# Optimization experiments

Hardware: AMD Instinct MI355X
Metric: run time of the kernel (lower is better)

## Reference

```python
import jax, jax.numpy as jnp
import numpy as np
from jax import lax

# pywt Wavelet('db3') analysis filters (dec_lo, dec_hi)
DEC_LO = jnp.array([0.035226291882100656, -0.08544127388224149, -0.13501102001039084,
                    0.4598775021193313, 0.8068915093133388, 0.3326705529509569], dtype=jnp.float32)
DEC_HI = jnp.array([-0.3326705529509569, 0.8068915093133388, -0.4598775021193313,
                    -0.13501102001039084, 0.08544127388224149, 0.035226291882100656], dtype=jnp.float32)


def _dwt_level(x):
    # One analysis level of pytorch_wavelets DWT1D with mode='zero'.
    # x: [B, N] -> (lo, hi) each [B, (N+L-1)//2]
    N = x.shape[-1]
    L = DEC_LO.shape[0]
    outsize = (N + L - 1) // 2  # pywt.dwt_coeff_len, zero mode
    p = 2 * (outsize - 1) - N + L
    # conv_general_dilated does cross-correlation; reversed filter == true convolution
    w = jnp.stack([DEC_LO[::-1], DEC_HI[::-1]])[:, None, :]  # [2, 1, L]
    y = lax.conv_general_dilated(x[:, None, :], w, window_strides=(2,),
                                 padding=[(p // 2, p - p // 2)])  # [B, 2, outsize]
    return y[:, 0, :], y[:, 1, :]


def _wavelet_features(sig, level=3):
    # sig: [B, N]. Returns (mean of final low-pass, sum over levels of ||hf||_2) per row.
    lo = sig
    high = jnp.zeros(sig.shape[0], sig.dtype)
    for _ in range(level):
        lo, hi = _dwt_level(lo)
        high = high + jnp.sqrt(jnp.sum(hi * hi, axis=-1))
    return jnp.mean(lo, axis=-1), high


def _dirichlet_weight(low, high):
    # Deterministic surrogate: Dirichlet([a1*10, a2*10]) has mean a1/(a1+a2),
    # replacing scipy dirichlet.rvs sampling with its expectation.
    a1 = jnp.clip(low, 1e-6)
    a2 = jnp.clip(high, 1e-6)
    return a1 / (a1 + a2)


def _forward(user_idx, item_idx, values, num_users, num_items):
    # item popularity: scatter-add of values * log1p(interaction count), L2-normalized
    counts = jnp.zeros(num_items, jnp.float32).at[item_idx].add(1.0)
    log_counts = jnp.log1p(counts)
    pop = jnp.zeros(num_items, jnp.float32).at[item_idx].add(values * log_counts[item_idx])
    pop = pop / (jnp.linalg.norm(pop) + 1e-8)
    # user activity
    act = jnp.zeros(num_users, jnp.float32).at[user_idx].add(
        values / jnp.log1p(pop[item_idx] + 1e-8))
    act = act / (jnp.linalg.norm(act) + 1e-8)
    # dense per-entity interaction signals (batched scatter replaces per-entity masking loop)
    user_sig = jnp.zeros((num_users, num_items), jnp.float32).at[user_idx, item_idx].add(values)
    user_sig = user_sig * (1.0 + act)[:, None]
    item_sig = jnp.zeros((num_items, num_users), jnp.float32).at[item_idx, user_idx].add(values)
    item_sig = item_sig * (1.0 + pop)[:, None]
    u_low, u_high = _wavelet_features(user_sig)
    i_low, i_high = _wavelet_features(item_sig)
    u_pop = _dirichlet_weight(u_low, u_high)
    i_pop = _dirichlet_weight(i_low, i_high)
    u_ni, i_ni = 1.0 - u_pop, 1.0 - i_pop
    wu_p, wu_n = u_pop[user_idx], u_ni[user_idx]
    wi_p, wi_n = i_pop[item_idx], i_ni[item_idx]
    # nnz-valued sparse outputs: [UIPG(=pop/pop), UING(=niche/niche), pop/niche, niche/pop]
    return jnp.stack([values * wu_p * wi_p,
                      values * wu_n * wi_n,
                      values * wu_p * wi_n,
                      values * wu_n * wi_p])


def setup_inputs():
    key = jax.random.key(0)
    k1, k2, k3 = jax.random.split(key, 3)
    NNZ, U, I = 2_000_000, 8192, 8192
    return {
        "user_idx": jax.random.randint(k1, (NNZ,), 0, U, dtype=jnp.int32),
        "item_idx": jax.random.randint(k2, (NNZ,), 0, I, dtype=jnp.int32),
        "values": jax.random.uniform(k3, (NNZ,), dtype=jnp.float32),
        "num_users": U,
        "num_items": I,
    }


def reference(user_idx, item_idx, values, num_users, num_items):
    return _forward(user_idx, item_idx, values, num_users, num_items)
```

## Files before the change

kernel.cpp:

```cpp
#include <hip/hip_runtime.h>
#include <math.h>

#define NE 8192
#define HT 1024
#define NCH 8
#define RT 512
#define NROWS 16

__device__ __constant__ float LO_R[6] = {
    0.3326705529509569f, 0.8068915093133388f, 0.4598775021193313f,
    -0.13501102001039084f, -0.08544127388224149f, 0.035226291882100656f};
__device__ __constant__ float HI_RV[6] = {
    0.035226291882100656f, 0.08544127388224149f, -0.13501102001039084f,
    -0.4598775021193313f, 0.8068915093133388f, -0.3326705529509569f};

__device__ __forceinline__ float4 blockReduce4(float a, float b, float c, float d,
                                               float (*red)[4]) {
    #pragma unroll
    for (int off = 32; off > 0; off >>= 1) {
        a += __shfl_down(a, off); b += __shfl_down(b, off);
        c += __shfl_down(c, off); d += __shfl_down(d, off);
    }
    int lane = threadIdx.x & 63, wid = threadIdx.x >> 6;
    if (lane == 0) { red[wid][0] = a; red[wid][1] = b; red[wid][2] = c; red[wid][3] = d; }
    __syncthreads();
    float4 r = make_float4(0.f, 0.f, 0.f, 0.f);
    if (threadIdx.x == 0) {
        int nw = blockDim.x >> 6;
        for (int w = 0; w < nw; ++w) {
            r.x += red[w][0]; r.y += red[w][1]; r.z += red[w][2]; r.w += red[w][3];
        }
    }
    return r;
}

__device__ __forceinline__ float blockReduceSum(float v, float* red) {
    #pragma unroll
    for (int off = 32; off > 0; off >>= 1) v += __shfl_down(v, off);
    int lane = threadIdx.x & 63, wid = threadIdx.x >> 6;
    if (lane == 0) red[wid] = v;
    __syncthreads();
    float r = 0.f;
    if (threadIdx.x == 0) {
        int nw = blockDim.x >> 6;
        for (int i = 0; i < nw; ++i) r += red[i];
    }
    return r;
}

__global__ void k_tables(float* __restrict__ resp, float4* __restrict__ Tdiag) {
    int a = blockIdx.x * blockDim.x + threadIdx.x;
    if (a >= NE) return;
    float lo1r[8], hi1r[8];
    int k1a = max(0, (a >> 1) - 3);
    #pragma unroll
    for (int t = 0; t < 8; ++t) {
        int k = k1a + t;
        int j = a - 2 * k + 4;
        bool ok = (j >= 0 && j <= 5 && k <= 4097);
        lo1r[t] = ok ? LO_R[j] : 0.f;
        hi1r[t] = ok ? HI_RV[j] : 0.f;
    }
    float lo2r[8], hi2r[8];
    int k2a = max(0, (k1a >> 1) - 1);
    #pragma unroll
    for (int t = 0; t < 8; ++t) {
        int k = k2a + t;
        float aL = 0.f, aH = 0.f;
        if (k <= 2050) {
            #pragma unroll
            for (int j = 0; j < 6; ++j) {
                int idx = 2 * k - 4 + j - k1a;
                if (idx >= 0 && idx < 8) {
                    aL = fmaf(LO_R[j], lo1r[idx], aL);
                    aH = fmaf(HI_RV[j], lo1r[idx], aH);
                }
            }
        }
        lo2r[t] = aL; hi2r[t] = aH;
    }
    float lo3r[8], hi3r[8];
    int k3a = max(0, (k2a >> 1) - 1);
    #pragma unroll
    for (int t = 0; t < 8; ++t) {
        int k = k3a + t;
        float aL = 0.f, aH = 0.f;
        if (k <= 1027) {
            #pragma unroll
            for (int j = 0; j < 6; ++j) {
                int idx = 2 * k - 4 + j - k2a;
                if (idx >= 0 && idx < 8) {
                    aL = fmaf(LO_R[j], lo2r[idx], aL);
                    aH = fmaf(HI_RV[j], lo2r[idx], aH);
                }
            }
        }
        lo3r[t] = aL; hi3r[t] = aH;
    }
    float g1 = 0.f, g2 = 0.f, g3 = 0.f, w3 = 0.f;
    #pragma unroll
    for (int t = 0; t < 8; ++t) {
        g1 = fmaf(hi1r[t], hi1r[t], g1);
        g2 = fmaf(hi2r[t], hi2r[t], g2);
        g3 = fmaf(hi3r[t], hi3r[t], g3);
        w3 += lo3r[t];
    }
    Tdiag[a] = make_float4(w3, g1, g2, g3);
    float* rp = resp + (size_t)a * 32;
    #pragma unroll
    for (int t = 0; t < 8; ++t) { rp[t] = hi1r[t]; rp[8 + t] = hi2r[t]; rp[16 + t] = hi3r[t]; }
    rp[24] = __int_as_float(k1a);
    rp[25] = __int_as_float(k2a);
    rp[26] = __int_as_float(k3a);
}

__global__ void k_gram(const float* __restrict__ resp, float* __restrict__ Gt) {
    int idx = blockIdx.x * 256 + threadIdx.x;
    if (idx >= NE * 35) return;
    int a = idx / 35;
    int d = idx - a * 35 + 1;
    int b = a + d;
    float v1 = 0.f, v2 = 0.f, v3 = 0.f;
    const float* ra = resp + (size_t)a * 32;
    if (b < NE) {
        const float* rb = resp + (size_t)b * 32;
        {
            int s = __float_as_int(rb[26]) - __float_as_int(ra[26]);
            #pragma unroll
            for (int u = 0; u < 8; ++u) {
                int t = u + s;
                if (t >= 0 && t < 8) v3 = fmaf(rb[16 + u], ra[16 + t], v3);
            }
        }
        if (d <= 15) {
            int s = __float_as_int(rb[25]) - __float_as_int(ra[25]);
            #pragma unroll
            for (int u = 0; u < 8; ++u) {
                int t = u + s;
                if (t >= 0 && t < 8) v2 = fmaf(rb[8 + u], ra[8 + t], v2);
            }
        }
        if (d <= 5) {
            int s = __float_as_int(rb[24]) - __float_as_int(ra[24]);
            #pragma unroll
            for (int u = 0; u < 8; ++u) {
                int t = u + s;
                if (t >= 0 && t < 8) v1 = fmaf(rb[u], ra[t], v1);
            }
        }
    }
    float* g = Gt + (size_t)a * 56;
    if (d <= 5)  g[d - 1] = v1;
    if (d <= 15) g[5 + d - 1] = v2;
    g[20 + d - 1] = v3;
}

__global__ __launch_bounds__(HT) void k_hist3(const int* __restrict__ ui,
                                              const int* __restrict__ ii,
                                              const float* __restrict__ v, int nnz,
                                              int* __restrict__ sliceU,
                                              int* __restrict__ sliceI,
                                              float* __restrict__ sliceS) {
    __shared__ int hU[NE];
    __shared__ int hI[NE];
    __shared__ float hS[NE];
    int b = blockIdx.x, tid = threadIdx.x, hb = gridDim.x;
    int4* hU4 = (int4*)hU; int4* hI4 = (int4*)hI; int4* hS4 = (int4*)hS;
    int4 z4 = make_int4(0, 0, 0, 0);
    for (int j = tid; j < NE / 4; j += HT) { hU4[j] = z4; hI4[j] = z4; hS4[j] = z4; }
    __syncthreads();
    int C = (nnz + hb - 1) / hb;
    int beg = b * C, end = min(nnz, beg + C);
    for (int n = beg + tid; n < end; n += HT) {
        atomicAdd(&hU[ui[n]], 1);
        int it = ii[n];
        atomicAdd(&hI[it], 1);
        atomicAdd(&hS[it], v[n]);
    }
    __syncthreads();
    size_t base = (size_t)b * NE;
    int4* sU = (int4*)(sliceU + base); int4* sI = (int4*)(sliceI + base);
    int4* sS = (int4*)(sliceS + base);
    for (int j = tid; j < NE / 4; j += HT) { sU[j] = hU4[j]; sI[j] = hI4[j]; sS[j] = hS4[j]; }
}

__global__ void k_chunksum3(const int* __restrict__ sliceU, const int* __restrict__ sliceI,
                            const float* __restrict__ sliceS, int spc,
                            int* __restrict__ csU, int* __restrict__ csI,
                            float* __restrict__ csS) {
    int i = blockIdx.x * 256 + threadIdx.x;
    int c = blockIdx.y;
    int b0 = c * spc;
    int cu = 0, ci = 0; float sv = 0.f;
    for (int b = b0; b < b0 + spc; ++b) {
        size_t o = (size_t)b * NE + i;
        cu += sliceU[o]; ci += sliceI[o]; sv += sliceS[o];
    }
    size_t oc = (size_t)c * NE + i;
    csU[oc] = cu; csI[oc] = ci; csS[oc] = sv;
}

__global__ void k_final3(const int* __restrict__ csU, const int* __restrict__ csI,
                         const float* __restrict__ csS,
                         int* cntU, int* cntI, float* popraw, float* normAcc) {
    __shared__ float red[4];
    int i = blockIdx.x * 256 + threadIdx.x;
    int cu = 0, ci = 0; float sv = 0.f;
    #pragma unroll
    for (int c = 0; c < NCH; ++c) {
        size_t o = (size_t)c * NE + i;
        cu += csU[o]; ci += csI[o]; sv += csS[o];
    }
    cntU[i] = cu; cntI[i] = ci;
    float p = log1pf((float)ci) * sv;
    popraw[i] = p;
    float s = blockReduceSum(p * p, red);
    if (threadIdx.x == 0) atomicAdd(&normAcc[0], s);
}

__global__ void k_scan2(const int* __restrict__ cntU, const int* __restrict__ cntI,
                        int* ptrU, int* ptrI) {
    __shared__ int sums[256];
    const int* cnt = blockIdx.x ? cntI : cntU;
    int* ptr = blockIdx.x ? ptrI : ptrU;
    int tid = threadIdx.x;
    int base = tid * 32;
    int local[32];
    int s = 0;
    #pragma unroll
    for (int j = 0; j < 32; ++j) { local[j] = cnt[base + j]; s += local[j]; }
    sums[tid] = s;
    __syncthreads();
    for (int off = 1; off < 256; off <<= 1) {
        int t = (tid >= off) ? sums[tid - off] : 0;
        __syncthreads();
        sums[tid] += t;
        __syncthreads();
    }
    int run = (tid > 0) ? sums[tid - 1] : 0;
    #pragma unroll
    for (int j = 0; j < 32; ++j) { ptr[base + j] = run; run += local[j]; }
    if (tid == 255) ptr[NE] = run;
}

__global__ void k_colscanB(int* csU, int* csI,
                           const int* __restrict__ ptrU, const int* __restrict__ ptrI) {
    int i = blockIdx.x * 256 + threadIdx.x;
    int* cs = blockIdx.y ? csI : csU;
    const int* ptr = blockIdx.y ? ptrI : ptrU;
    int run = ptr[i];
    #pragma unroll
    for (int c = 0; c < NCH; ++c) {
        size_t o = (size_t)c * NE + i;
        int t = cs[o]; cs[o] = run; run += t;
    }
}

__global__ void k_colscanC(int* sliceU, int* sliceI,
                           const int* __restrict__ csU, const int* __restrict__ csI, int spc) {
    int i = blockIdx.x * 256 + threadIdx.x;
    int c = blockIdx.y;
    int* slice = blockIdx.z ? sliceI : sliceU;
    const int* cs = blockIdx.z ? csI : csU;
    int run = cs[(size_t)c * NE + i];
    int b0 = c * spc;
    for (int b = b0; b < b0 + spc; ++b) {
        size_t o = (size_t)b * NE + i;
        int t = slice[o]; slice[o] = run; run += t;
    }
}

__global__ __launch_bounds__(HT) void k_scatter2(const int* __restrict__ ui,
                                                 const int* __restrict__ ii,
                                                 const float* __restrict__ v, int nnz,
                                                 const int* __restrict__ sliceU,
                                                 const int* __restrict__ sliceI,
                                                 const float* __restrict__ popraw,
                                                 const float* __restrict__ normAcc,
                                                 int2* __restrict__ pairsU,
                                                 int2* __restrict__ pairsI,
                                                 float* __restrict__ sliceA) {
    __shared__ int curU[NE];
    __shared__ int curI[NE];
    __shared__ float hA[NE];
    int b = blockIdx.x, tid = threadIdx.x, hb = gridDim.x;
    const int4* sU = (const int4*)(sliceU + (size_t)b * NE);
    const int4* sI = (const int4*)(sliceI + (size_t)b * NE);
    int4* cU4 = (int4*)curU; int4* cI4 = (int4*)curI;
    float4* hA4 = (float4*)hA;
    float4 zf = make_float4(0.f, 0.f, 0.f, 0.f);
    for (int j = tid; j < NE / 4; j += HT) { cU4[j] = sU[j]; cI4[j] = sI[j]; hA4[j] = zf; }
    __syncthreads();
    float rs0 = 1.f / (sqrtf(normAcc[0]) + 1e-8f);
    int C = (nnz + hb - 1) / hb;
    int beg = b * C, end = min(nnz, beg + C);
    for (int n = beg + tid; n < end; n += HT) {
        int u = ui[n], it = ii[n];
        float val = v[n];
        atomicAdd(&hA[u], val / log1pf(popraw[it] * rs0 + 1e-8f));
        int pU = atomicAdd(&curU[u], 1);
        pairsU[pU] = make_int2(it, __float_as_int(val));
        int pI = atomicAdd(&curI[it], 1);
        pairsI[pI] = make_int2(u, __float_as_int(val));
    }
    __syncthreads();
    float4* sA = (float4*)(sliceA + (size_t)b * NE);
    for (int j = tid; j < NE / 4; j += HT) sA[j] = hA4[j];
}

__global__ void k_actchunk(const float* __restrict__ sliceA, int spc, float* __restrict__ csA) {
    int i = blockIdx.x * 256 + threadIdx.x;
    int c = blockIdx.y;
    int b0 = c * spc;
    float a = 0.f;
    for (int b = b0; b < b0 + spc; ++b) a += sliceA[(size_t)b * NE + i];
    csA[(size_t)c * NE + i] = a;
}

__global__ void k_actfinal(const float* __restrict__ csA, float* act, float* normAcc) {
    __shared__ float red[4];
    int i = blockIdx.x * 256 + threadIdx.x;
    float a = 0.f;
    #pragma unroll
    for (int c = 0; c < NCH; ++c) a += csA[(size_t)c * NE + i];
    act[i] = a;
    float s = blockReduceSum(a * a, red);
    if (threadIdx.x == 0) atomicAdd(&normAcc[1], s);
}

__device__ __forceinline__ void scan_one(int p, float v,
                                         const float* __restrict__ X,
                                         const unsigned int* __restrict__ M,
                                         const float4* __restrict__ Tdiag,
                                         const float* __restrict__ Gt,
                                         float& s1, float& s2, float& s3, float& ls) {
    float xp = X[p];
    float4 td = Tdiag[p];
    ls = fmaf(v, td.x, ls);
    float vx = v * xp;
    s1 = fmaf(vx, td.y, s1);
    s2 = fmaf(vx, td.z, s2);
    s3 = fmaf(vx, td.w, s3);
    int w = p >> 5, sh = (p & 31) + 1;
    unsigned long long lo64 = (unsigned long long)M[w] |
                              ((unsigned long long)M[w + 1] << 32);
    unsigned long long win = (lo64 >> sh) |
                             ((unsigned long long)M[w + 2] << (64 - sh));
    win &= (1ull << 35) - 1ull;
    const float* g = Gt + (size_t)p * 56;
    while (win) {
        int d = __ffsll((unsigned long long)win);
        win &= win - 1;
        float c = 2.f * v * X[p + d];
        s3 = fmaf(c, g[19 + d], s3);
        if (d <= 15) s2 = fmaf(c, g[4 + d], s2);
        if (d <= 5)  s1 = fmaf(c, g[d - 1], s1);
    }
}

__global__ __launch_bounds__(RT) void k_rows(const int* __restrict__ ptrU,
                                             const int* __restrict__ ptrI,
                                             const int2* __restrict__ pairsU,
                                             const int2* __restrict__ pairsI,
                                             const float* __restrict__ popraw,
                                             const float* __restrict__ actraw,
                                             const float* __restrict__ normAcc,
                                             const float4* __restrict__ Tdiag,
                                             const float* __restrict__ Gt,
                                             float* __restrict__ u_w,
                                             float* __restrict__ i_w) {
    __shared__ __align__(16) float X[NE];
    __shared__ unsigned int M[260];
    __shared__ float red[RT / 64][4];
    int tid = threadIdx.x;
    int bid = blockIdx.x;
    bool isUser = bid >= 512;
    int r0 = (isUser ? bid - 512 : bid) * NROWS;
    const int* ptr = isUser ? ptrU : ptrI;
    const int2* pairs = isUser ? pairsU : pairsI;
    const float* raw = isUser ? actraw : popraw;
    float* w_out = isUser ? u_w : i_w;
    float rs = 1.f / (sqrtf(normAcc[isUser ? 1 : 0]) + 1e-8f);

    float4* X4 = (float4*)X;
    const float4 z4 = make_float4(0.f, 0.f, 0.f, 0.f);
    for (int q = tid; q < NE / 4; q += RT) X4[q] = z4;
    if (tid < 260) M[tid] = 0u;

    int beg = ptr[r0], end = ptr[r0 + 1];
    int2 pr = make_int2(0, 0);
    if (tid < end - beg) pr = pairs[beg + tid];

    for (int j = 0; j < NROWS; ++j) {
        int rl = r0 + j;
        float rawv = raw[rl];
        __syncthreads();

        int cnt = end - beg;
        if (tid < cnt) {
            int p = pr.x;
            atomicAdd(&X[p], __int_as_float(pr.y));
            atomicOr(&M[p >> 5], 1u << (p & 31));
        }
        for (int n = beg + RT + tid; n < end; n += RT) {
            int2 q2 = pairs[n];
            atomicAdd(&X[q2.x], __int_as_float(q2.y));
            atomicOr(&M[q2.x >> 5], 1u << (q2.x & 31));
        }
        __syncthreads();

        float s1 = 0.f, s2 = 0.f, s3 = 0.f, ls = 0.f;
        if (tid < cnt)
            scan_one(pr.x, __int_as_float(pr.y), X, M, Tdiag, Gt, s1, s2, s3, ls);
        for (int n = beg + RT + tid; n < end; n += RT) {
            int2 q2 = pairs[n];
            scan_one(q2.x, __int_as_float(q2.y), X, M, Tdiag, Gt, s1, s2, s3, ls);
        }

        int begN = end, endN = end;
        int2 prN = make_int2(0, 0);
        if (j + 1 < NROWS) {
            endN = ptr[rl + 2];
            prN = pairs[begN + tid];
        }
        __syncthreads();

        if (tid < cnt) { X[pr.x] = 0.f; M[pr.x >> 5] = 0u; }
        for (int n = beg + RT + tid; n < end; n += RT) {
            int2 q2 = pairs[n];
            X[q2.x] = 0.f; M[q2.x >> 5] = 0u;
        }

        float4 t = blockReduce4(s1, s2, s3, ls, red);
        if (tid == 0) {
            float sc = 1.f + rawv * rs;
            float high = (sqrtf(fmaxf(t.x, 0.f)) + sqrtf(fmaxf(t.y, 0.f)) +
                          sqrtf(fmaxf(t.z, 0.f))) * sc;
            float low = t.w * (1.f / 1028.f) * sc;
            float a1 = fmaxf(low, 1e-6f);
            float a2 = fmaxf(high, 1e-6f);
            w_out[rl] = a1 / (a1 + a2);
        }
        beg = begN; end = endN; pr = prN;
    }
}

__global__ void k_out(const int* __restrict__ ui, const int* __restrict__ ii,
                      const float* __restrict__ v, int nnz,
                      const float* __restrict__ u_w, const float* __restrict__ i_w,
                      float* __restrict__ out) {
    int ngroups = nnz >> 2;
    int idx = blockIdx.x * blockDim.x + threadIdx.x;
    int stride = gridDim.x * blockDim.x;
    const int4* ui4 = (const int4*)ui;
    const int4* ii4 = (const int4*)ii;
    const float4* v4 = (const float4*)v;
    float4* o0 = (float4*)out;
    float4* o1 = (float4*)(out + (size_t)nnz);
    float4* o2 = (float4*)(out + 2 * (size_t)nnz);
    float4* o3 = (float4*)(out + 3 * (size_t)nnz);
    for (int g = idx; g < ngroups; g += stride) {
        int4 u = ui4[g];
        int4 it = ii4[g];
        float4 val = v4[g];
        float wu0 = u_w[u.x], wu1 = u_w[u.y], wu2 = u_w[u.z], wu3 = u_w[u.w];
        float wi0 = i_w[it.x], wi1 = i_w[it.y], wi2 = i_w[it.z], wi3 = i_w[it.w];
        o0[g] = make_float4(val.x * wu0 * wi0, val.y * wu1 * wi1,
                            val.z * wu2 * wi2, val.w * wu3 * wi3);
        o1[g] = make_float4(val.x * (1.f - wu0) * (1.f - wi0), val.y * (1.f - wu1) * (1.f - wi1),
                            val.z * (1.f - wu2) * (1.f - wi2), val.w * (1.f - wu3) * (1.f - wi3));
        o2[g] = make_float4(val.x * wu0 * (1.f - wi0), val.y * wu1 * (1.f - wi1),
                            val.z * wu2 * (1.f - wi2), val.w * wu3 * (1.f - wi3));
        o3[g] = make_float4(val.x * (1.f - wu0) * wi0, val.y * (1.f - wu1) * wi1,
                            val.z * (1.f - wu2) * wi2, val.w * (1.f - wu3) * wi3);
    }
    int tail = ngroups * 4;
    for (int n = tail + idx; n < nnz; n += stride) {
        float val = v[n];
        float wu = u_w[ui[n]], wi = i_w[ii[n]];
        out[n] = val * wu * wi;
        out[(size_t)nnz + n] = val * (1.f - wu) * (1.f - wi);
        out[2 * (size_t)nnz + n] = val * wu * (1.f - wi);
        out[3 * (size_t)nnz + n] = val * (1.f - wu) * wi;
    }
}

extern "C" void kernel_launch(void* const* d_in, const int* in_sizes, int n_in,
                              void* d_out, int out_size, void* d_ws, size_t ws_size,
                              hipStream_t stream) {
    const int* ui = (const int*)d_in[0];
    const int* ii = (const int*)d_in[1];
    const float* vals = (const float*)d_in[2];
    int nnz = in_sizes[0];
    float* out = (float*)d_out;

    char* ws = (char*)d_ws;
    size_t off = 0;
    auto take = [&](size_t bytes) -> char* {
        char* p = ws + off;
        off = (off + bytes + 255) & ~(size_t)255;
        return p;
    };

    int*   cntU    = (int*)take(NE * 4);
    int*   cntI    = (int*)take(NE * 4);
    float* popraw  = (float*)take(NE * 4);
    float* actraw  = (float*)take(NE * 4);
    int*   ptrU    = (int*)take((NE + 1) * 4);
    int*   ptrI    = (int*)take((NE + 1) * 4);
    float* u_w     = (float*)take(NE * 4);
    float* i_w     = (float*)take(NE * 4);
    float* normAcc = (float*)take(256);
    float4* Tdiag  = (float4*)take((size_t)NE * 16);
    float* Gt      = (float*)take((size_t)NE * 56 * 4);
    float* resp    = (float*)take((size_t)NE * 32 * 4);
    int*   csU     = (int*)take((size_t)NCH * NE * 4);
    int*   csI     = (int*)take((size_t)NCH * NE * 4);
    float* csS     = (float*)take((size_t)NCH * NE * 4);
    int2*  pairsU  = (int2*)take((size_t)nnz * 8);
    int2*  pairsI  = (int2*)take((size_t)nnz * 8);
    size_t fixedEnd = off;

    int hb = 256;
    while (hb > 8 && fixedEnd + 3 * (size_t)hb * NE * 4 + 4096 > ws_size) hb >>= 1;
    int spc = hb / NCH;
    int*   sliceU = (int*)take((size_t)hb * NE * 4);
    int*   sliceI = (int*)take((size_t)hb * NE * 4);
    float* sliceS = (float*)take((size_t)hb * NE * 4);

    hipMemsetAsync(normAcc, 0, 256, stream);

    int nb = (nnz / 4 + 255) / 256;
    if (nb > 2048) nb = 2048;

    k_tables<<<NE / 64, 64, 0, stream>>>(resp, Tdiag);
    k_gram<<<(NE * 35 + 255) / 256, 256, 0, stream>>>(resp, Gt);

    k_hist3<<<hb, HT, 0, stream>>>(ui, ii, vals, nnz, sliceU, sliceI, sliceS);
    k_chunksum3<<<dim3(32, NCH), 256, 0, stream>>>(sliceU, sliceI, sliceS, spc, csU, csI, csS);
    k_final3<<<32, 256, 0, stream>>>(csU, csI, csS, cntU, cntI, popraw, normAcc);

    k_scan2<<<2, 256, 0, stream>>>(cntU, cntI, ptrU, ptrI);
    k_colscanB<<<dim3(32, 2), 256, 0, stream>>>(csU, csI, ptrU, ptrI);
    k_colscanC<<<dim3(32, NCH, 2), 256, 0, stream>>>(sliceU, sliceI, csU, csI, spc);

    k_scatter2<<<hb, HT, 0, stream>>>(ui, ii, vals, nnz, sliceU, sliceI,
                                      popraw, normAcc, pairsU, pairsI, sliceS);

    k_actchunk<<<dim3(32, NCH), 256, 0, stream>>>(sliceS, spc, csS);
    k_actfinal<<<32, 256, 0, stream>>>(csS, actraw, normAcc);

    k_rows<<<1024, RT, 0, stream>>>(ptrU, ptrI, pairsU, pairsI,
                                    popraw, actraw, normAcc, Tdiag, Gt, u_w, i_w);

    k_out<<<nb, 256, 0, stream>>>(ui, ii, vals, nnz, u_w, i_w, out);
}
```

Baseline: 251.1 us.

## Replace per-row block reduction with shared atomics and prefetch Tdiag

```diff
diff --git a/kernel.cpp b/kernel.cpp
--- a/kernel.cpp
+++ b/kernel.cpp
@@ -13,26 +13,6 @@
 __device__ __constant__ float HI_RV[6] = {
     0.035226291882100656f, 0.08544127388224149f, -0.13501102001039084f,
     -0.4598775021193313f, 0.8068915093133388f, -0.3326705529509569f};
-
-__device__ __forceinline__ float4 blockReduce4(float a, float b, float c, float d,
-                                               float (*red)[4]) {
-    #pragma unroll
-    for (int off = 32; off > 0; off >>= 1) {
-        a += __shfl_down(a, off); b += __shfl_down(b, off);
-        c += __shfl_down(c, off); d += __shfl_down(d, off);
-    }
-    int lane = threadIdx.x & 63, wid = threadIdx.x >> 6;
-    if (lane == 0) { red[wid][0] = a; red[wid][1] = b; red[wid][2] = c; red[wid][3] = d; }
-    __syncthreads();
-    float4 r = make_float4(0.f, 0.f, 0.f, 0.f);
-    if (threadIdx.x == 0) {
-        int nw = blockDim.x >> 6;
-        for (int w = 0; w < nw; ++w) {
-            r.x += red[w][0]; r.y += red[w][1]; r.z += red[w][2]; r.w += red[w][3];
-        }
-    }
-    return r;
-}
 
 __device__ __forceinline__ float blockReduceSum(float v, float* red) {
     #pragma unroll
@@ -328,14 +308,12 @@
     if (threadIdx.x == 0) atomicAdd(&normAcc[1], s);
 }
 
-__device__ __forceinline__ void scan_one(int p, float v,
+__device__ __forceinline__ void scan_one(int p, float v, float4 td,
                                          const float* __restrict__ X,
                                          const unsigned int* __restrict__ M,
-                                         const float4* __restrict__ Tdiag,
                                          const float* __restrict__ Gt,
                                          float& s1, float& s2, float& s3, float& ls) {
     float xp = X[p];
-    float4 td = Tdiag[p];
     ls = fmaf(v, td.x, ls);
     float vx = v * xp;
     s1 = fmaf(vx, td.y, s1);
@@ -371,7 +349,7 @@
                                              float* __restrict__ i_w) {
     __shared__ __align__(16) float X[NE];
     __shared__ unsigned int M[260];
-    __shared__ float red[RT / 64][4];
+    __shared__ float acc[NROWS][4];
     int tid = threadIdx.x;
     int bid = blockIdx.x;
     bool isUser = bid >= 512;
@@ -386,14 +364,18 @@
     const float4 z4 = make_float4(0.f, 0.f, 0.f, 0.f);
     for (int q = tid; q < NE / 4; q += RT) X4[q] = z4;
     if (tid < 260) M[tid] = 0u;
+    if (tid < NROWS * 4) ((float*)acc)[tid] = 0.f;
 
     int beg = ptr[r0], end = ptr[r0 + 1];
     int2 pr = make_int2(0, 0);
-    if (tid < end - beg) pr = pairs[beg + tid];
+    float4 td = z4;
+    if (tid < end - beg) {
+        pr = pairs[beg + tid];
+        td = Tdiag[pr.x];
+    }
 
     for (int j = 0; j < NROWS; ++j) {
         int rl = r0 + j;
-        float rawv = raw[rl];
         __syncthreads();
 
         int cnt = end - beg;
@@ -409,19 +391,37 @@
         }
         __syncthreads();
 
+        int begN = end, endN = end;
+        int2 prN = make_int2(0, 0);
+        float4 tdN = z4;
+        if (j + 1 < NROWS) {
+            endN = ptr[rl + 2];
+            if (tid < endN - begN) {
+                prN = pairs[begN + tid];
+                tdN = Tdiag[prN.x];
+            }
+        }
+
         float s1 = 0.f, s2 = 0.f, s3 = 0.f, ls = 0.f;
         if (tid < cnt)
-            scan_one(pr.x, __int_as_float(pr.y), X, M, Tdiag, Gt, s1, s2, s3, ls);
+            scan_one(pr.x, __int_as_float(pr.y), td, X, M, Gt, s1, s2, s3, ls);
         for (int n = beg + RT + tid; n < end; n += RT) {
             int2 q2 = pairs[n];
-            scan_one(q2.x, __int_as_float(q2.y), X, M, Tdiag, Gt, s1, s2, s3, ls);
-        }
-
-        int begN = end, endN = end;
-        int2 prN = make_int2(0, 0);
-        if (j + 1 < NROWS) {
-            endN = ptr[rl + 2];
-            prN = pairs[begN + tid];
+            scan_one(q2.x, __int_as_float(q2.y), Tdiag[q2.x], X, M, Gt, s1, s2, s3, ls);
+        }
+
+        #pragma unroll
+        for (int off = 32; off > 0; off >>= 1) {
+            s1 += __shfl_down(s1, off);
+            s2 += __shfl_down(s2, off);
+            s3 += __shfl_down(s3, off);
+            ls += __shfl_down(ls, off);
+        }
+        if ((tid & 63) == 0) {
+            atomicAdd(&acc[j][0], s1);
+            atomicAdd(&acc[j][1], s2);
+            atomicAdd(&acc[j][2], s3);
+            atomicAdd(&acc[j][3], ls);
         }
         __syncthreads();
 
@@ -430,18 +430,20 @@
             int2 q2 = pairs[n];
             X[q2.x] = 0.f; M[q2.x >> 5] = 0u;
         }
-
-        float4 t = blockReduce4(s1, s2, s3, ls, red);
-        if (tid == 0) {
-            float sc = 1.f + rawv * rs;
-            float high = (sqrtf(fmaxf(t.x, 0.f)) + sqrtf(fmaxf(t.y, 0.f)) +
-                          sqrtf(fmaxf(t.z, 0.f))) * sc;
-            float low = t.w * (1.f / 1028.f) * sc;
-            float a1 = fmaxf(low, 1e-6f);
-            float a2 = fmaxf(high, 1e-6f);
-            w_out[rl] = a1 / (a1 + a2);
-        }
-        beg = begN; end = endN; pr = prN;
+        beg = begN; end = endN; pr = prN; td = tdN;
+    }
+
+    __syncthreads();
+    if (tid < NROWS) {
+        float t1 = acc[tid][0], t2 = acc[tid][1], t3 = acc[tid][2], tl = acc[tid][3];
+        float rawv = raw[r0 + tid];
+        float sc = 1.f + rawv * rs;
+        float high = (sqrtf(fmaxf(t1, 0.f)) + sqrtf(fmaxf(t2, 0.f)) +
+                      sqrtf(fmaxf(t3, 0.f))) * sc;
+        float low = tl * (1.f / 1028.f) * sc;
+        float a1 = fmaxf(low, 1e-6f);
+        float a2 = fmaxf(high, 1e-6f);
+        w_out[r0 + tid] = a1 / (a1 + a2);
     }
 }
 
```

Result: faster. 239.5 us (-4.6%).
